# Kernel tuning notes

Hardware: AMD Instinct MI355X
Metric: run time of the kernel (lower is better)

Reference implementation:

```python
import jax, jax.numpy as jnp
import numpy as np

COMMITMENT_COST = 0.25


def setup_inputs() -> dict:
    key = jax.random.key(0)
    k1, k2 = jax.random.split(key)
    x = jax.random.normal(k1, (32, 64, 64, 64), dtype=jnp.float32)  # NCHW, C=embedding_dim
    # nn.Embedding weight init: uniform(-1/num_embeddings, 1/num_embeddings)
    codebook = jax.random.uniform(k2, (512, 64), dtype=jnp.float32,
                                  minval=-1.0 / 512.0, maxval=1.0 / 512.0)
    return {"x": x, "codebook": codebook}


def reference(x, codebook):
    # NCHW -> NHWC
    inputs = jnp.transpose(x, (0, 2, 3, 1))  # [B,H,W,D]
    B, H, W, D = inputs.shape
    flat = inputs.reshape(-1, D)  # [N,D]
    # Squared Euclidean distances (argmin identical to torch.cdist's sqrt'ed distances)
    d2 = (jnp.sum(flat * flat, axis=1, keepdims=True)
          - 2.0 * flat @ codebook.T
          + jnp.sum(codebook * codebook, axis=1)[None, :])  # [N,K]
    idx = jnp.argmin(d2, axis=1)  # [N]
    quantized = codebook[idx].reshape(B, H, W, D)
    e_latent_loss = jnp.mean((jax.lax.stop_gradient(quantized) - inputs) ** 2)
    q_latent_loss = jnp.mean((quantized - jax.lax.stop_gradient(inputs)) ** 2)
    c_loss = q_latent_loss + COMMITMENT_COST * e_latent_loss
    # Straight-through estimator
    quantized = inputs + jax.lax.stop_gradient(quantized - inputs)
    quantized = jnp.transpose(quantized, (0, 3, 1, 2))  # NHWC -> NCHW
    return c_loss, quantized
```

## Files before the change

### kernel.cpp

```cpp
#include <hip/hip_runtime.h>
#include <hip/hip_bf16.h>
#include <hip/hip_fp8.h>


typedef __attribute__((ext_vector_type(4))) float f32x4;

#define WS_CBF   0
#define WS_HN2   32768
#define WS_RED   34816

#define K_XA   0
#define K_HN   4096
#define K_IDX  17408
#define K_SZ   17664

__device__ __forceinline__ unsigned f2b1(float f) {
  unsigned u = __float_as_uint(f);
  return (u + 0x7FFFu + ((u >> 16) & 1)) >> 16;
}
__device__ __forceinline__ unsigned pack2(float lo, float hi) {
  return f2b1(lo) | (f2b1(hi) << 16);
}

#if defined(__has_builtin)
#  if __has_builtin(__builtin_amdgcn_cvt_pk_fp8_f32)
#    define HAVE_CVT_PK_FP8 1
#  endif
#endif
__device__ __forceinline__ unsigned cvt4_fp8(float a, float b, float c, float d) {
#ifdef HAVE_CVT_PK_FP8
  int v = __builtin_amdgcn_cvt_pk_fp8_f32(a, b, 0, false);
  v = __builtin_amdgcn_cvt_pk_fp8_f32(c, d, v, true);
  return (unsigned)v;
#else
  __hip_fp8_e4m3 fa(a), fb(b), fc(c), fd(d);
  return (unsigned)fa.__x | ((unsigned)fb.__x << 8) |
         ((unsigned)fc.__x << 16) | ((unsigned)fd.__x << 24);
#endif
}

__global__ void vq_prep(const float* __restrict__ cb, char* __restrict__ ws) {
  const int n = blockIdx.x * 64 + threadIdx.x;
  const float4* cb4 = (const float4*)cb;
  float4 f[16];
  #pragma unroll
  for (int j = 0; j < 16; ++j) f[j] = cb4[(n << 4) + j];
  float s = 0.f;
  #pragma unroll
  for (int j = 0; j < 16; ++j)
    s += f[j].x * f[j].x + f[j].y * f[j].y + f[j].z * f[j].z + f[j].w * f[j].w;
  ((float*)(ws + WS_HN2))[n] = 256.0f - 128.0f * s;
  const int ct = n >> 4, col = n & 15;
  #pragma unroll
  for (int kk = 0; kk < 2; ++kk) {
    #pragma unroll
    for (int g = 0; g < 4; ++g) {
      float4 a = f[kk * 8 + g * 2], b = f[kk * 8 + g * 2 + 1];
      uint2 u;
      u.x = cvt4_fp8(a.x * 256.f, a.y * 256.f, a.z * 256.f, a.w * 256.f);
      u.y = cvt4_fp8(b.x * 256.f, b.y * 256.f, b.z * 256.f, b.w * 256.f);
      *(uint2*)(ws + WS_CBF + (((ct << 1) + kk) << 9) + (((g << 4) | col) << 3)) = u;
    }
  }
}

__global__ void __launch_bounds__(128, 4)
vq_main(const float* __restrict__ x, const float* __restrict__ cb,
        const char* __restrict__ wsr, float* __restrict__ out,
        float* __restrict__ wsw) {
  __shared__ __align__(16) char smem[K_SZ];
  char*  xaz  = smem + K_XA;
  float* hn2z = (float*)(smem + K_HN);
  int*   idxz = (int*)(smem + K_IDX);
  float* qld2 = (float*)smem;

  const int t    = threadIdx.x;
  const int bid  = blockIdx.x;
  const int bimg = bid >> 6;
  const int hw0  = (bid & 63) << 6;
  const float4* xb4 = (const float4*)(x + (bimg << 18) + hw0);
  const float4* cb4 = (const float4*)cb;
  const long*   cbl = (const long*)(wsr + WS_CBF);

  float xsq = 0.f;
  {
    const int q = t >> 3;
    const int c = t & 7;
    #pragma unroll
    for (int j = 0; j < 2; ++j) {
      const int f = c + (j << 3);
      float4 A0 = xb4[((4 * q + 0) << 10) + f];
      float4 A1 = xb4[((4 * q + 1) << 10) + f];
      float4 A2 = xb4[((4 * q + 2) << 10) + f];
      float4 A3 = xb4[((4 * q + 3) << 10) + f];
      xsq += A0.x*A0.x + A0.y*A0.y + A0.z*A0.z + A0.w*A0.w;
      xsq += A1.x*A1.x + A1.y*A1.y + A1.z*A1.z + A1.w*A1.w;
      xsq += A2.x*A2.x + A2.y*A2.y + A2.z*A2.z + A2.w*A2.w;
      xsq += A3.x*A3.x + A3.y*A3.y + A3.z*A3.z + A3.w*A3.w;
      const float* a0 = (const float*)&A0;
      const float* a1 = (const float*)&A1;
      const float* a2 = (const float*)&A2;
      const float* a3 = (const float*)&A3;
      #pragma unroll
      for (int u = 0; u < 4; ++u) {
        int r = (f << 2) + u;
        unsigned pk = cvt4_fp8(a0[u], a1[u], a2[u], a3[u]);
        *(unsigned*)(xaz + r * 64 + ((q << 2) ^ ((r & 7) << 3))) = pk;
      }
    }
  }
  #pragma unroll
  for (int i = 0; i < 4; ++i)
    hn2z[t + (i << 7)] = ((const float*)(wsr + WS_HN2))[t + (i << 7)];
  __syncthreads();

  const int lane = t & 63;
  const int wid  = t >> 6;
  const int lrow = lane & 15;
  const int hb   = (lane >> 4) << 3;

  long af[2][2];
  #pragma unroll
  for (int s = 0; s < 2; ++s) {
    int row = (wid << 5) + (s << 4) + lrow;
    int sw = (row & 7) << 3;
    af[s][0] = *(const long*)(xaz + row * 64 + (hb ^ sw));
    af[s][1] = *(const long*)(xaz + row * 64 + ((32 | hb) ^ sw));
  }

  unsigned bestu[2][4];
  #pragma unroll
  for (int s = 0; s < 2; ++s)
    #pragma unroll
    for (int r = 0; r < 4; ++r) bestu[s][r] = 0u;

  const unsigned tag0 = 511u - (unsigned)lrow;

  #pragma unroll 2
  for (int ct = 0; ct < 32; ++ct) {
    const long b0 = cbl[(ct << 7) + lane];
    const long b1 = cbl[(ct << 7) + 64 + lane];
    const float hv = hn2z[(ct << 4) + lrow];
    const unsigned tag = tag0 - (unsigned)(ct << 4);
    #pragma unroll
    for (int s = 0; s < 2; ++s) {
      f32x4 acc = {hv, hv, hv, hv};
      acc = __builtin_amdgcn_mfma_f32_16x16x32_fp8_fp8(af[s][0], b0, acc, 0, 0, 0);
      acc = __builtin_amdgcn_mfma_f32_16x16x32_fp8_fp8(af[s][1], b1, acc, 0, 0, 0);
      #pragma unroll
      for (int r = 0; r < 4; ++r) {
        unsigned key = (__float_as_uint(acc[r]) & 0xFFFFFE00u) | tag;
        bestu[s][r] = max(bestu[s][r], key);
      }
    }
  }

  float vsum = 0.f;
  #pragma unroll
  for (int s = 0; s < 2; ++s) {
    #pragma unroll
    for (int r = 0; r < 4; ++r) {
      unsigned k = bestu[s][r];
      #pragma unroll
      for (int m = 1; m <= 8; m <<= 1) k = max(k, (unsigned)__shfl_xor(k, m, 64));
      if (lrow == 0) {
        idxz[(wid << 5) + (s << 4) + ((lane >> 4) << 2) + r] =
            (int)(511u - (k & 511u));
        vsum += fmaf(__uint_as_float(k & 0xFFFFFE00u), 1.0f / 256.0f, -1.0f);
      }
    }
  }
  float lacc = xsq - 2.0f * vsum;
  #pragma unroll
  for (int m = 32; m; m >>= 1) lacc += __shfl_xor(lacc, m, 64);
  if (lane == 0) wsw[(bid << 1) + wid] = lacc;
  __syncthreads();

  {
    const int myrow = t >> 1;
    const int chh   = t & 1;
    const int myidx = idxz[myrow];
    const float4* cbr = cb4 + (myidx << 4) + (chh << 3);
    #pragma unroll
    for (int j = 0; j < 8; ++j) {
      float4 v = cbr[j];
      const int d = (chh << 5) + (j << 2);
      qld2[(d + 0) * 68 + myrow] = v.x;
      qld2[(d + 1) * 68 + myrow] = v.y;
      qld2[(d + 2) * 68 + myrow] = v.z;
      qld2[(d + 3) * 68 + myrow] = v.w;
    }
  }
  __syncthreads();
  {
    float* outq = out + 1 + (bimg << 18) + hw0;
    const int r4 = (t & 15) << 2;
    const int d0 = t >> 4;
    #pragma unroll
    for (int i = 0; i < 8; ++i) {
      const int d = d0 + (i << 3);
      float4 v = *(const float4*)(qld2 + d * 68 + r4);
      *(float4*)(outq + (d << 12) + r4) = v;
    }
  }
}

__global__ void vq_finalize(const float* __restrict__ ws, float* __restrict__ out) {
  int t = threadIdx.x;
  __shared__ float red[4];
  float v = 0.f;
  #pragma unroll
  for (int k = 0; k < 16; ++k) v += ws[t + (k << 8)];
  #pragma unroll
  for (int m = 32; m; m >>= 1) v += __shfl_xor(v, m, 64);
  if ((t & 63) == 0) red[t >> 6] = v;
  __syncthreads();
  if (t == 0) out[0] = (red[0] + red[1] + red[2] + red[3]) * (1.25f / 8388608.0f);
}

extern "C" void kernel_launch(void* const* d_in, const int* in_sizes, int n_in,
                              void* d_out, int out_size, void* d_ws, size_t ws_size,
                              hipStream_t stream) {
  const float* x  = (const float*)d_in[0];
  const float* cb = (const float*)d_in[1];
  float* out = (float*)d_out;
  char*  ws  = (char*)d_ws;
  vq_prep<<<8, 64, 0, stream>>>(cb, ws);
  vq_main<<<2048, 128, 0, stream>>>(x, cb, ws, out, (float*)(ws + WS_RED));
  vq_finalize<<<1, 256, 0, stream>>>((float*)(ws + WS_RED), out);
}
```

Before: 33.13 us.

## Split VQ into argmin and channel-sliced scatter kernels, fuse loss finalize

The main kernel now only computes argmin indices (stored as uint16 in workspace) and partial losses, which frees most of its shared memory. A new scatter kernel loads one image's indices and a four-channel slice of the codebook into LDS and writes the NCHW output with coalesced float4 stores. Block 0 of the scatter kernel also does the loss reduction, which removes the separate finalize launch. The cost is an extra round trip of the indices through global memory in exchange for higher occupancy in the argmin kernel and cheaper output writes.

```diff
diff --git a/kernel.cpp b/kernel.cpp
--- a/kernel.cpp
+++ b/kernel.cpp
@@ -8,11 +8,7 @@
 #define WS_CBF   0
 #define WS_HN2   32768
 #define WS_RED   34816
-
-#define K_XA   0
-#define K_HN   4096
-#define K_IDX  17408
-#define K_SZ   17664
+#define WS_IDX   51200
 
 __device__ __forceinline__ unsigned f2b1(float f) {
   unsigned u = __float_as_uint(f);
@@ -65,22 +61,17 @@
 }
 
 __global__ void __launch_bounds__(128, 4)
-vq_main(const float* __restrict__ x, const float* __restrict__ cb,
-        const char* __restrict__ wsr, float* __restrict__ out,
-        float* __restrict__ wsw) {
-  __shared__ __align__(16) char smem[K_SZ];
-  char*  xaz  = smem + K_XA;
-  float* hn2z = (float*)(smem + K_HN);
-  int*   idxz = (int*)(smem + K_IDX);
-  float* qld2 = (float*)smem;
+vq_argmin(const float* __restrict__ x, char* __restrict__ ws) {
+  __shared__ __align__(16) char smem[6144];
+  char*  xaz  = smem;
+  float* hn2z = (float*)(smem + 4096);
 
   const int t    = threadIdx.x;
   const int bid  = blockIdx.x;
   const int bimg = bid >> 6;
   const int hw0  = (bid & 63) << 6;
   const float4* xb4 = (const float4*)(x + (bimg << 18) + hw0);
-  const float4* cb4 = (const float4*)cb;
-  const long*   cbl = (const long*)(wsr + WS_CBF);
+  const long*   cbl = (const long*)(ws + WS_CBF);
 
   float xsq = 0.f;
   {
@@ -111,7 +102,7 @@
   }
   #pragma unroll
   for (int i = 0; i < 4; ++i)
-    hn2z[t + (i << 7)] = ((const float*)(wsr + WS_HN2))[t + (i << 7)];
+    hn2z[t + (i << 7)] = ((const float*)(ws + WS_HN2))[t + (i << 7)];
   __syncthreads();
 
   const int lane = t & 63;
@@ -155,6 +146,7 @@
     }
   }
 
+  unsigned short* wsid = (unsigned short*)(ws + WS_IDX);
   float vsum = 0.f;
   #pragma unroll
   for (int s = 0; s < 2; ++s) {
@@ -164,8 +156,8 @@
       #pragma unroll
       for (int m = 1; m <= 8; m <<= 1) k = max(k, (unsigned)__shfl_xor(k, m, 64));
       if (lrow == 0) {
-        idxz[(wid << 5) + (s << 4) + ((lane >> 4) << 2) + r] =
-            (int)(511u - (k & 511u));
+        const int row = (wid << 5) + (s << 4) + ((lane >> 4) << 2) + r;
+        wsid[(bid << 6) + row] = (unsigned short)(511u - (k & 511u));
         vsum += fmaf(__uint_as_float(k & 0xFFFFFE00u), 1.0f / 256.0f, -1.0f);
       }
     }
@@ -173,49 +165,60 @@
   float lacc = xsq - 2.0f * vsum;
   #pragma unroll
   for (int m = 32; m; m >>= 1) lacc += __shfl_xor(lacc, m, 64);
-  if (lane == 0) wsw[(bid << 1) + wid] = lacc;
+  if (lane == 0) ((float*)(ws + WS_RED))[(bid << 1) + wid] = lacc;
+}
+
+__global__ void __launch_bounds__(256, 2)
+vq_scatter(const float* __restrict__ cb, const char* __restrict__ ws,
+           float* __restrict__ out) {
+  __shared__ __align__(16) unsigned short idxl[4096];
+  __shared__ __align__(16) float cbtl[4][512];
+  __shared__ float redl[4];
+  const int t   = threadIdx.x;
+  const int b   = blockIdx.x;
+  const int img = b >> 4;
+  const int dbase = (b & 15) << 2;
+
+  {
+    const uint4* ig = (const uint4*)(ws + WS_IDX + (img << 13));
+    ((uint4*)idxl)[t]       = ig[t];
+    ((uint4*)idxl)[t + 256] = ig[t + 256];
+  }
+  {
+    const int c0 = t << 1;
+    float4 v0 = *(const float4*)(cb + (c0 << 6) + dbase);
+    float4 v1 = *(const float4*)(cb + ((c0 + 1) << 6) + dbase);
+    cbtl[0][c0] = v0.x; cbtl[1][c0] = v0.y;
+    cbtl[2][c0] = v0.z; cbtl[3][c0] = v0.w;
+    cbtl[0][c0 + 1] = v1.x; cbtl[1][c0 + 1] = v1.y;
+    cbtl[2][c0 + 1] = v1.z; cbtl[3][c0 + 1] = v1.w;
+  }
+  if (b == 0) {
+    const float* red = (const float*)(ws + WS_RED);
+    float v = 0.f;
+    #pragma unroll
+    for (int k = 0; k < 16; ++k) v += red[t + (k << 8)];
+    #pragma unroll
+    for (int m = 32; m; m >>= 1) v += __shfl_xor(v, m, 64);
+    if ((t & 63) == 0) redl[t >> 6] = v;
+  }
   __syncthreads();
-
-  {
-    const int myrow = t >> 1;
-    const int chh   = t & 1;
-    const int myidx = idxz[myrow];
-    const float4* cbr = cb4 + (myidx << 4) + (chh << 3);
-    #pragma unroll
-    for (int j = 0; j < 8; ++j) {
-      float4 v = cbr[j];
-      const int d = (chh << 5) + (j << 2);
-      qld2[(d + 0) * 68 + myrow] = v.x;
-      qld2[(d + 1) * 68 + myrow] = v.y;
-      qld2[(d + 2) * 68 + myrow] = v.z;
-      qld2[(d + 3) * 68 + myrow] = v.w;
-    }
-  }
-  __syncthreads();
-  {
-    float* outq = out + 1 + (bimg << 18) + hw0;
-    const int r4 = (t & 15) << 2;
-    const int d0 = t >> 4;
-    #pragma unroll
-    for (int i = 0; i < 8; ++i) {
-      const int d = d0 + (i << 3);
-      float4 v = *(const float4*)(qld2 + d * 68 + r4);
-      *(float4*)(outq + (d << 12) + r4) = v;
-    }
-  }
-}
-
-__global__ void vq_finalize(const float* __restrict__ ws, float* __restrict__ out) {
-  int t = threadIdx.x;
-  __shared__ float red[4];
-  float v = 0.f;
-  #pragma unroll
-  for (int k = 0; k < 16; ++k) v += ws[t + (k << 8)];
-  #pragma unroll
-  for (int m = 32; m; m >>= 1) v += __shfl_xor(v, m, 64);
-  if ((t & 63) == 0) red[t >> 6] = v;
-  __syncthreads();
-  if (t == 0) out[0] = (red[0] + red[1] + red[2] + red[3]) * (1.25f / 8388608.0f);
+  if (b == 0 && t == 0)
+    out[0] = (redl[0] + redl[1] + redl[2] + redl[3]) * (1.25f / 8388608.0f);
+
+  float* ob = out + 1 + (img << 18) + (dbase << 12);
+  #pragma unroll
+  for (int j = 0; j < 4; ++j) {
+    const float* cp = cbtl[j];
+    float* op = ob + (j << 12);
+    #pragma unroll
+    for (int cc = 0; cc < 4; ++cc) {
+      const int r0 = ((cc << 8) + t) << 2;
+      float4 v = {cp[idxl[r0 + 0]], cp[idxl[r0 + 1]],
+                  cp[idxl[r0 + 2]], cp[idxl[r0 + 3]]};
+      *(float4*)(op + r0) = v;
+    }
+  }
 }
 
 extern "C" void kernel_launch(void* const* d_in, const int* in_sizes, int n_in,
@@ -226,6 +229,6 @@
   float* out = (float*)d_out;
   char*  ws  = (char*)d_ws;
   vq_prep<<<8, 64, 0, stream>>>(cb, ws);
-  vq_main<<<2048, 128, 0, stream>>>(x, cb, ws, out, (float*)(ws + WS_RED));
-  vq_finalize<<<1, 256, 0, stream>>>((float*)(ws + WS_RED), out);
-}
+  vq_argmin<<<2048, 128, 0, stream>>>(x, ws);
+  vq_scatter<<<512, 256, 0, stream>>>(cb, ws, out);
+}
```

Result: slower. 33.93 us (+2.4%).
